# Kernel optimization log

Measured on AMD Instinct MI355X. Metric: run time of the kernel, lower is better.

Reference implementation:

```python
import jax, jax.numpy as jnp
import numpy as np

B, S, D, KC = 32, 4096, 64, 256  # batch*heads, seq_len, head_dim, compressed dim


def setup_inputs() -> dict:
    key = jax.random.key(0)
    ks = jax.random.split(key, 7)
    return {
        "Q": jax.random.normal(ks[0], (B, S, D), dtype=jnp.float32),
        "K": jax.random.normal(ks[1], (B, S, D), dtype=jnp.float32),
        "V": jax.random.normal(ks[2], (B, S, D), dtype=jnp.float32),
        "E_w": jax.random.normal(ks[3], (KC, S), dtype=jnp.float32) * (1.0 / np.sqrt(S)),
        "E_b": jax.random.normal(ks[4], (KC,), dtype=jnp.float32) * 0.01,
        "F_w": jax.random.normal(ks[5], (KC, S), dtype=jnp.float32) * (1.0 / np.sqrt(S)),
        "F_b": jax.random.normal(ks[6], (KC,), dtype=jnp.float32) * 0.01,
    }


def reference(Q, K, V, E_w, E_b, F_w, F_b):
    # K: [B,S,D] -> transpose -> [B,D,S]; E proj over seq axis -> [B,D,KC]
    Ke = jnp.einsum("bsd,ks->bdk", K, E_w) + E_b  # [B, D, KC]
    # scores: Q @ E(K) -> [B, S, KC], scaled by sqrt(head_dim)
    scale = jnp.sqrt(jnp.asarray(D, dtype=Q.dtype))
    P = jnp.einsum("bsd,bdk->bsk", Q, Ke) / scale
    # causal mask: torch.triu(ones(S, KC)) keeps (i, j) where j >= i
    i = jnp.arange(S)[:, None]
    j = jnp.arange(KC)[None, :]
    keep = j >= i  # [S, KC]
    P = jnp.where(keep[None, :, :], P, jnp.asarray(-1e10, dtype=P.dtype))
    P = jax.nn.softmax(P, axis=-1)  # dropout p=0.0 -> identity
    # V: [B,S,D] -> [B,D,S]; F proj -> [B,D,KC]; transpose -> [B,KC,D]
    Vf = jnp.einsum("bsd,ks->bkd", V, F_w) + F_b[None, :, None]  # [B, KC, D]
    out = jnp.einsum("bsk,bkd->bsd", P, Vf)  # [B, S, D]
    return out
```

## Files before the change

kernel.cpp:

```cpp
#include <hip/hip_runtime.h>
#include <hip/hip_bf16.h>
#include <math.h>

#define NB  32
#define NS  4096
#define ND  64
#define NKC 256

#define BK   128
#define ASA  132
#define ASB  132

#define QSTR  72
#define PBSTR 264
#define VSTR  264

typedef __attribute__((ext_vector_type(8))) short short8;
typedef __attribute__((ext_vector_type(4))) float f32x4;

__device__ __forceinline__ short f2bf(float f) {
    union { float f; unsigned u; } v; v.f = f;
    return (short)((v.u + 0x7FFFu + ((v.u >> 16) & 1u)) >> 16);
}

__global__ __launch_bounds__(256) void prep(
    const float* __restrict__ Ew, const float* __restrict__ Fw,
    short* __restrict__ EwB, short* __restrict__ FwB)
{
    const int gid = blockIdx.x * 256 + threadIdx.x;
    const int half = (NKC * NS) / 8;
    const float* src = (gid < half) ? Ew : Fw;
    short* dst       = (gid < half) ? EwB : FwB;
    const int i8 = (gid < half) ? gid : gid - half;
    float4 a = *(const float4*)&src[(size_t)i8 * 8];
    float4 c = *(const float4*)&src[(size_t)i8 * 8 + 4];
    short8 w;
    w[0] = f2bf(a.x); w[1] = f2bf(a.y); w[2] = f2bf(a.z); w[3] = f2bf(a.w);
    w[4] = f2bf(c.x); w[5] = f2bf(c.y); w[6] = f2bf(c.z); w[7] = f2bf(c.w);
    *(short8*)&dst[(size_t)i8 * 8] = w;
}

template <typename AT>
__global__ __launch_bounds__(256) void proj_gemm(
    const AT* __restrict__ EwX, const AT* __restrict__ FwX,
    const float* __restrict__ K, const float* __restrict__ V,
    float* __restrict__ KeT, float* __restrict__ Vf)
{
    const int bid = blockIdx.x;
    const int r8 = bid & 7, mt = (bid >> 3) & 3, G = bid >> 5;
    const int g  = G * 8 + r8, b = g >> 1, mm = g & 1;

    const AT* __restrict__ Ab    = mm ? FwX : EwX;
    const float* __restrict__ Bg = mm ? V   : K;
    float* __restrict__ Cout     = mm ? Vf  : KeT;

    const int t = threadIdx.x, wave = t >> 6, lane = t & 63;
    const int lm = lane & 15, g4 = lane >> 4;
    __shared__ short As[64 * ASA];
    __shared__ short Bs[64 * ASB];
    const size_t bBase = (size_t)b * NS * ND;
    const size_t aBase = (size_t)mt * 64 * NS;
    const int rA = t >> 4, jA = t & 15;
    const int dB = t & 31, sB = t >> 5;

    f32x4 acc[4];
#pragma unroll
    for (int nt = 0; nt < 4; ++nt) acc[nt] = (f32x4){0.f, 0.f, 0.f, 0.f};

    short8 pa[4];
    float4 paf[8];
    float2 pb[16];

#pragma unroll
    for (int i = 0; i < 4; ++i) {
        if constexpr (sizeof(AT) == 2) {
            pa[i] = *(const short8*)&Ab[aBase + (size_t)(i * 16 + rA) * NS + jA * 8];
        } else {
            paf[2 * i]     = *(const float4*)&Ab[aBase + (size_t)(i * 16 + rA) * NS + jA * 8];
            paf[2 * i + 1] = *(const float4*)&Ab[aBase + (size_t)(i * 16 + rA) * NS + jA * 8 + 4];
        }
    }
#pragma unroll
    for (int h = 0; h < 2; ++h)
#pragma unroll
        for (int i = 0; i < 8; ++i)
            pb[h * 8 + i] = *(const float2*)&Bg[bBase + (size_t)(h * 64 + sB * 8 + i) * ND + dB * 2];

    for (int s0 = 0; s0 < NS; s0 += BK) {
#pragma unroll
        for (int i = 0; i < 4; ++i) {
            if constexpr (sizeof(AT) == 2) {
                *(short8*)&As[(i * 16 + rA) * ASA + jA * 8] = pa[i];
            } else {
                short8 w;
                w[0] = f2bf(paf[2 * i].x);     w[1] = f2bf(paf[2 * i].y);
                w[2] = f2bf(paf[2 * i].z);     w[3] = f2bf(paf[2 * i].w);
                w[4] = f2bf(paf[2 * i + 1].x); w[5] = f2bf(paf[2 * i + 1].y);
                w[6] = f2bf(paf[2 * i + 1].z); w[7] = f2bf(paf[2 * i + 1].w);
                *(short8*)&As[(i * 16 + rA) * ASA + jA * 8] = w;
            }
        }
#pragma unroll
        for (int h = 0; h < 2; ++h) {
            short8 w0, w1;
#pragma unroll
            for (int i = 0; i < 8; ++i) {
                w0[i] = f2bf(pb[h * 8 + i].x);
                w1[i] = f2bf(pb[h * 8 + i].y);
            }
            *(short8*)&Bs[(dB * 2 + 0) * ASB + h * 64 + sB * 8] = w0;
            *(short8*)&Bs[(dB * 2 + 1) * ASB + h * 64 + sB * 8] = w1;
        }
        __syncthreads();

        if (s0 + BK < NS) {
            const int sn = s0 + BK;
#pragma unroll
            for (int i = 0; i < 4; ++i) {
                if constexpr (sizeof(AT) == 2) {
                    pa[i] = *(const short8*)&Ab[aBase + (size_t)(i * 16 + rA) * NS + sn + jA * 8];
                } else {
                    paf[2 * i]     = *(const float4*)&Ab[aBase + (size_t)(i * 16 + rA) * NS + sn + jA * 8];
                    paf[2 * i + 1] = *(const float4*)&Ab[aBase + (size_t)(i * 16 + rA) * NS + sn + jA * 8 + 4];
                }
            }
#pragma unroll
            for (int h = 0; h < 2; ++h)
#pragma unroll
                for (int i = 0; i < 8; ++i)
                    pb[h * 8 + i] = *(const float2*)&Bg[bBase + (size_t)(sn + h * 64 + sB * 8 + i) * ND + dB * 2];
        }

#pragma unroll
        for (int ks = 0; ks < BK; ks += 32) {
            short8 aF = *(const short8*)&As[(wave * 16 + lm) * ASA + ks + g4 * 8];
#pragma unroll
            for (int nt = 0; nt < 4; ++nt) {
                short8 bF = *(const short8*)&Bs[(nt * 16 + lm) * ASB + ks + g4 * 8];
                acc[nt] = __builtin_amdgcn_mfma_f32_16x16x32_bf16(aF, bF, acc[nt], 0, 0, 0);
            }
        }
        __syncthreads();
    }

#pragma unroll
    for (int nt = 0; nt < 4; ++nt)
#pragma unroll
        for (int rr = 0; rr < 4; ++rr) {
            int kc = mt * 64 + wave * 16 + g4 * 4 + rr;
            Cout[((size_t)b * NKC + kc) * ND + nt * 16 + lm] = acc[nt][rr];
        }
}

__global__ __launch_bounds__(256) void attn_fused(
    const float* __restrict__ Q,  const float* __restrict__ KeT,
    const float* __restrict__ Vf, const float* __restrict__ Eb,
    const float* __restrict__ Fb, float* __restrict__ out)
{
    const int x = blockIdx.x, b = blockIdx.y, t = threadIdx.x;

    if (x >= 8) {
        __shared__ float pq[16][64];
        __shared__ float mv[64];
        const int kg = t >> 4, dq = t & 15;
        float4 s4 = (float4){0.f, 0.f, 0.f, 0.f};
        for (int p = 0; p < 16; ++p) {
            int k = p * 16 + kg;
            float4 v = *(const float4*)&Vf[((size_t)b * NKC + k) * ND + dq * 4];
            float fb = Fb[k];
            s4.x += v.x + fb; s4.y += v.y + fb; s4.z += v.z + fb; s4.w += v.w + fb;
        }
        *(float4*)&pq[kg][dq * 4] = s4;
        __syncthreads();
        if (t < 64) {
            float m = 0.f;
#pragma unroll
            for (int i = 0; i < 16; ++i) m += pq[i][t];
            mv[t] = m * (1.f / 256.f);
        }
        __syncthreads();
        const int r0 = 256 + (x - 8) * 64;
#pragma unroll
        for (int i = 0; i < 4; ++i) {
            int idx = i * 256 + t, row = idx >> 4, q = idx & 15;
            *(float4*)&out[((size_t)b * NS + r0 + row) * ND + q * 4] =
                *(const float4*)&mv[q * 4];
        }
        return;
    }

    const int s0 = x * 32;
    const int wave = t >> 6, lane = t & 63, lm = lane & 15, g = lane >> 4;
    __shared__ short Qs[32 * QSTR];
    __shared__ short PsB[32 * PBSTR];
    __shared__ short VfT[64 * VSTR];
    __shared__ float rsums[32][4];

    {
        int row = t >> 3, dq = t & 7;
        size_t off = ((size_t)b * NS + s0 + row) * ND + dq * 8;
        float4 q0 = *(const float4*)&Q[off], q1 = *(const float4*)&Q[off + 4];
        short8 w;
        w[0] = f2bf(q0.x); w[1] = f2bf(q0.y); w[2] = f2bf(q0.z); w[3] = f2bf(q0.w);
        w[4] = f2bf(q1.x); w[5] = f2bf(q1.y); w[6] = f2bf(q1.z); w[7] = f2bf(q1.w);
        *(short8*)&Qs[row * QSTR + dq * 8] = w;
    }
    {
        const int dB = t & 31, sB = t >> 5;
#pragma unroll
        for (int pass = 0; pass < 4; ++pass) {
            int kb = pass * 64 + sB * 8;
            float2 v[8]; float fb[8];
#pragma unroll
            for (int i = 0; i < 8; ++i) {
                v[i]  = *(const float2*)&Vf[((size_t)b * NKC + kb + i) * ND + dB * 2];
                fb[i] = Fb[kb + i];
            }
            short8 w0, w1;
#pragma unroll
            for (int i = 0; i < 8; ++i) {
                w0[i] = f2bf(v[i].x + fb[i]);
                w1[i] = f2bf(v[i].y + fb[i]);
            }
            *(short8*)&VfT[(dB * 2 + 0) * VSTR + kb] = w0;
            *(short8*)&VfT[(dB * 2 + 1) * VSTR + kb] = w1;
        }
    }
    __syncthreads();

    f32x4 accP[2][4];
#pragma unroll
    for (int rt = 0; rt < 2; ++rt)
#pragma unroll
        for (int kk = 0; kk < 4; ++kk) accP[rt][kk] = (f32x4){0.f, 0.f, 0.f, 0.f};
#pragma unroll
    for (int kk = 0; kk < 4; ++kk) {
        int kt = wave * 4 + kk;
        float ebv = Eb[kt * 16 + lm];
#pragma unroll
        for (int ks2 = 0; ks2 < 2; ++ks2) {
            const float* kp = &KeT[((size_t)b * NKC + kt * 16 + lm) * ND + ks2 * 32 + g * 8];
            float4 c0 = *(const float4*)kp, c1 = *(const float4*)(kp + 4);
            short8 bf;
            bf[0] = f2bf(c0.x + ebv); bf[1] = f2bf(c0.y + ebv);
            bf[2] = f2bf(c0.z + ebv); bf[3] = f2bf(c0.w + ebv);
            bf[4] = f2bf(c1.x + ebv); bf[5] = f2bf(c1.y + ebv);
            bf[6] = f2bf(c1.z + ebv); bf[7] = f2bf(c1.w + ebv);
#pragma unroll
            for (int rt = 0; rt < 2; ++rt) {
                short8 aq = *(const short8*)&Qs[(rt * 16 + lm) * QSTR + ks2 * 32 + g * 8];
                accP[rt][kk] = __builtin_amdgcn_mfma_f32_16x16x32_bf16(aq, bf, accP[rt][kk], 0, 0, 0);
            }
        }
    }
#pragma unroll
    for (int rt = 0; rt < 2; ++rt)
#pragma unroll
        for (int r = 0; r < 4; ++r) {
            float s = 0.f;
            int rowg = s0 + rt * 16 + g * 4 + r;
#pragma unroll
            for (int kk = 0; kk < 4; ++kk) {
                int col = wave * 64 + kk * 16 + lm;
                float e = (col >= rowg) ? __expf(accP[rt][kk][r] * 0.125f) : 0.f;
                accP[rt][kk][r] = e;
                s += e;
            }
#pragma unroll
            for (int off = 1; off <= 8; off <<= 1) s += __shfl_xor(s, off, 64);
            if (lm == 0) rsums[rt * 16 + g * 4 + r][wave] = s;
        }
    __syncthreads();
#pragma unroll
    for (int rt = 0; rt < 2; ++rt)
#pragma unroll
        for (int r = 0; r < 4; ++r) {
            float4 rs = *(const float4*)&rsums[rt * 16 + g * 4 + r][0];
            float inv = 1.f / (rs.x + rs.y + rs.z + rs.w);
#pragma unroll
            for (int kk = 0; kk < 4; ++kk)
                PsB[(rt * 16 + g * 4 + r) * PBSTR + wave * 64 + kk * 16 + lm] =
                    f2bf(accP[rt][kk][r] * inv);
        }
    __syncthreads();

    f32x4 oa[2];
    oa[0] = (f32x4){0.f, 0.f, 0.f, 0.f};
    oa[1] = (f32x4){0.f, 0.f, 0.f, 0.f};
    for (int ks = x; ks < 8; ++ks) {
        short8 bv = *(const short8*)&VfT[(wave * 16 + lm) * VSTR + ks * 32 + g * 8];
#pragma unroll
        for (int rt = 0; rt < 2; ++rt) {
            short8 av = *(const short8*)&PsB[(rt * 16 + lm) * PBSTR + ks * 32 + g * 8];
            oa[rt] = __builtin_amdgcn_mfma_f32_16x16x32_bf16(av, bv, oa[rt], 0, 0, 0);
        }
    }
#pragma unroll
    for (int rt = 0; rt < 2; ++rt)
#pragma unroll
        for (int r = 0; r < 4; ++r)
            out[((size_t)b * NS + s0 + rt * 16 + g * 4 + r) * ND + wave * 16 + lm] = oa[rt][r];
}

extern "C" void kernel_launch(void* const* d_in, const int* in_sizes, int n_in,
                              void* d_out, int out_size, void* d_ws, size_t ws_size,
                              hipStream_t stream) {
    (void)in_sizes; (void)n_in; (void)out_size;
    const float* Q  = (const float*)d_in[0];
    const float* K  = (const float*)d_in[1];
    const float* V  = (const float*)d_in[2];
    const float* Ew = (const float*)d_in[3];
    const float* Eb = (const float*)d_in[4];
    const float* Fw = (const float*)d_in[5];
    const float* Fb = (const float*)d_in[6];
    float* out = (float*)d_out;

    const size_t nKe = (size_t)NB * NKC * ND;
    float* KeT = (float*)d_ws;
    float* Vf  = KeT + nKe;

    if (ws_size >= 8u * 1024 * 1024) {
        short* EwB = (short*)(Vf + nKe);
        short* FwB = EwB + (size_t)NKC * NS;
        prep<<<dim3(1024), 256, 0, stream>>>(Ew, Fw, EwB, FwB);
        proj_gemm<short><<<dim3(256), 256, 0, stream>>>(EwB, FwB, K, V, KeT, Vf);
    } else {
        proj_gemm<float><<<dim3(256), 256, 0, stream>>>(Ew, Fw, K, V, KeT, Vf);
    }
    attn_fused<<<dim3(68, NB), 256, 0, stream>>>(Q, KeT, Vf, Eb, Fb, out);
}
```

Before: 195.3 us.

## Retile projection GEMM into 32x64 tiles with 512-thread blocks

The projection GEMM now has each block compute a 32-row slice of the compressed dimension instead of 64. Blocks grow to 512 threads (8 waves), and each wave owns a single 16x16 output tile. The grid doubles to 512 blocks, which raises parallelism and occupancy and shrinks per-thread register state. The cost is that each K/V chunk is loaded and converted to bf16 by twice as many blocks, and each wave issues only one MFMA per shared-memory fragment load.

```diff
diff --git a/kernel.cpp b/kernel.cpp
--- a/kernel.cpp
+++ b/kernel.cpp
@@ -41,13 +41,13 @@
 }
 
 template <typename AT>
-__global__ __launch_bounds__(256) void proj_gemm(
+__global__ __launch_bounds__(512, 4) void proj_gemm(
     const AT* __restrict__ EwX, const AT* __restrict__ FwX,
     const float* __restrict__ K, const float* __restrict__ V,
     float* __restrict__ KeT, float* __restrict__ Vf)
 {
     const int bid = blockIdx.x;
-    const int r8 = bid & 7, mt = (bid >> 3) & 3, G = bid >> 5;
+    const int r8 = bid & 7, mt = (bid >> 3) & 7, G = bid >> 6;
     const int g  = G * 8 + r8, b = g >> 1, mm = g & 1;
 
     const AT* __restrict__ Ab    = mm ? FwX : EwX;
@@ -56,100 +56,77 @@
 
     const int t = threadIdx.x, wave = t >> 6, lane = t & 63;
     const int lm = lane & 15, g4 = lane >> 4;
-    __shared__ short As[64 * ASA];
+    const int kcT = wave & 1, dT = wave >> 1;
+    __shared__ short As[32 * ASA];
     __shared__ short Bs[64 * ASB];
     const size_t bBase = (size_t)b * NS * ND;
-    const size_t aBase = (size_t)mt * 64 * NS;
+    const size_t aBase = (size_t)mt * 32 * NS;
     const int rA = t >> 4, jA = t & 15;
     const int dB = t & 31, sB = t >> 5;
 
-    f32x4 acc[4];
-#pragma unroll
-    for (int nt = 0; nt < 4; ++nt) acc[nt] = (f32x4){0.f, 0.f, 0.f, 0.f};
-
-    short8 pa[4];
-    float4 paf[8];
-    float2 pb[16];
-
-#pragma unroll
-    for (int i = 0; i < 4; ++i) {
+    f32x4 acc = (f32x4){0.f, 0.f, 0.f, 0.f};
+
+    short8 pa;
+    float4 paf[2];
+    float2 pb[8];
+
+    if constexpr (sizeof(AT) == 2) {
+        pa = *(const short8*)&Ab[aBase + (size_t)rA * NS + jA * 8];
+    } else {
+        paf[0] = *(const float4*)&Ab[aBase + (size_t)rA * NS + jA * 8];
+        paf[1] = *(const float4*)&Ab[aBase + (size_t)rA * NS + jA * 8 + 4];
+    }
+#pragma unroll
+    for (int i = 0; i < 8; ++i)
+        pb[i] = *(const float2*)&Bg[bBase + (size_t)(sB * 8 + i) * ND + dB * 2];
+
+    for (int s0 = 0; s0 < NS; s0 += BK) {
         if constexpr (sizeof(AT) == 2) {
-            pa[i] = *(const short8*)&Ab[aBase + (size_t)(i * 16 + rA) * NS + jA * 8];
+            *(short8*)&As[rA * ASA + jA * 8] = pa;
         } else {
-            paf[2 * i]     = *(const float4*)&Ab[aBase + (size_t)(i * 16 + rA) * NS + jA * 8];
-            paf[2 * i + 1] = *(const float4*)&Ab[aBase + (size_t)(i * 16 + rA) * NS + jA * 8 + 4];
-        }
-    }
-#pragma unroll
-    for (int h = 0; h < 2; ++h)
-#pragma unroll
-        for (int i = 0; i < 8; ++i)
-            pb[h * 8 + i] = *(const float2*)&Bg[bBase + (size_t)(h * 64 + sB * 8 + i) * ND + dB * 2];
-
-    for (int s0 = 0; s0 < NS; s0 += BK) {
-#pragma unroll
-        for (int i = 0; i < 4; ++i) {
-            if constexpr (sizeof(AT) == 2) {
-                *(short8*)&As[(i * 16 + rA) * ASA + jA * 8] = pa[i];
-            } else {
-                short8 w;
-                w[0] = f2bf(paf[2 * i].x);     w[1] = f2bf(paf[2 * i].y);
-                w[2] = f2bf(paf[2 * i].z);     w[3] = f2bf(paf[2 * i].w);
-                w[4] = f2bf(paf[2 * i + 1].x); w[5] = f2bf(paf[2 * i + 1].y);
-                w[6] = f2bf(paf[2 * i + 1].z); w[7] = f2bf(paf[2 * i + 1].w);
-                *(short8*)&As[(i * 16 + rA) * ASA + jA * 8] = w;
-            }
-        }
-#pragma unroll
-        for (int h = 0; h < 2; ++h) {
+            short8 w;
+            w[0] = f2bf(paf[0].x); w[1] = f2bf(paf[0].y);
+            w[2] = f2bf(paf[0].z); w[3] = f2bf(paf[0].w);
+            w[4] = f2bf(paf[1].x); w[5] = f2bf(paf[1].y);
+            w[6] = f2bf(paf[1].z); w[7] = f2bf(paf[1].w);
+            *(short8*)&As[rA * ASA + jA * 8] = w;
+        }
+        {
             short8 w0, w1;
 #pragma unroll
-            for (int i = 0; i < 8; ++i) {
-                w0[i] = f2bf(pb[h * 8 + i].x);
-                w1[i] = f2bf(pb[h * 8 + i].y);
-            }
-            *(short8*)&Bs[(dB * 2 + 0) * ASB + h * 64 + sB * 8] = w0;
-            *(short8*)&Bs[(dB * 2 + 1) * ASB + h * 64 + sB * 8] = w1;
+            for (int i = 0; i < 8; ++i) { w0[i] = f2bf(pb[i].x); w1[i] = f2bf(pb[i].y); }
+            *(short8*)&Bs[(dB * 2 + 0) * ASB + sB * 8] = w0;
+            *(short8*)&Bs[(dB * 2 + 1) * ASB + sB * 8] = w1;
         }
         __syncthreads();
 
         if (s0 + BK < NS) {
             const int sn = s0 + BK;
-#pragma unroll
-            for (int i = 0; i < 4; ++i) {
-                if constexpr (sizeof(AT) == 2) {
-                    pa[i] = *(const short8*)&Ab[aBase + (size_t)(i * 16 + rA) * NS + sn + jA * 8];
-                } else {
-                    paf[2 * i]     = *(const float4*)&Ab[aBase + (size_t)(i * 16 + rA) * NS + sn + jA * 8];
-                    paf[2 * i + 1] = *(const float4*)&Ab[aBase + (size_t)(i * 16 + rA) * NS + sn + jA * 8 + 4];
-                }
-            }
-#pragma unroll
-            for (int h = 0; h < 2; ++h)
-#pragma unroll
-                for (int i = 0; i < 8; ++i)
-                    pb[h * 8 + i] = *(const float2*)&Bg[bBase + (size_t)(sn + h * 64 + sB * 8 + i) * ND + dB * 2];
+            if constexpr (sizeof(AT) == 2) {
+                pa = *(const short8*)&Ab[aBase + (size_t)rA * NS + sn + jA * 8];
+            } else {
+                paf[0] = *(const float4*)&Ab[aBase + (size_t)rA * NS + sn + jA * 8];
+                paf[1] = *(const float4*)&Ab[aBase + (size_t)rA * NS + sn + jA * 8 + 4];
+            }
+#pragma unroll
+            for (int i = 0; i < 8; ++i)
+                pb[i] = *(const float2*)&Bg[bBase + (size_t)(sn + sB * 8 + i) * ND + dB * 2];
         }
 
 #pragma unroll
         for (int ks = 0; ks < BK; ks += 32) {
-            short8 aF = *(const short8*)&As[(wave * 16 + lm) * ASA + ks + g4 * 8];
-#pragma unroll
-            for (int nt = 0; nt < 4; ++nt) {
-                short8 bF = *(const short8*)&Bs[(nt * 16 + lm) * ASB + ks + g4 * 8];
-                acc[nt] = __builtin_amdgcn_mfma_f32_16x16x32_bf16(aF, bF, acc[nt], 0, 0, 0);
-            }
+            short8 aF = *(const short8*)&As[(kcT * 16 + lm) * ASA + ks + g4 * 8];
+            short8 bF = *(const short8*)&Bs[(dT * 16 + lm) * ASB + ks + g4 * 8];
+            acc = __builtin_amdgcn_mfma_f32_16x16x32_bf16(aF, bF, acc, 0, 0, 0);
         }
         __syncthreads();
     }
 
 #pragma unroll
-    for (int nt = 0; nt < 4; ++nt)
-#pragma unroll
-        for (int rr = 0; rr < 4; ++rr) {
-            int kc = mt * 64 + wave * 16 + g4 * 4 + rr;
-            Cout[((size_t)b * NKC + kc) * ND + nt * 16 + lm] = acc[nt][rr];
-        }
+    for (int rr = 0; rr < 4; ++rr) {
+        int kc = mt * 32 + kcT * 16 + g4 * 4 + rr;
+        Cout[((size_t)b * NKC + kc) * ND + dT * 16 + lm] = acc[rr];
+    }
 }
 
 __global__ __launch_bounds__(256) void attn_fused(
@@ -323,9 +300,9 @@
         short* EwB = (short*)(Vf + nKe);
         short* FwB = EwB + (size_t)NKC * NS;
         prep<<<dim3(1024), 256, 0, stream>>>(Ew, Fw, EwB, FwB);
-        proj_gemm<short><<<dim3(256), 256, 0, stream>>>(EwB, FwB, K, V, KeT, Vf);
+        proj_gemm<short><<<dim3(512), 512, 0, stream>>>(EwB, FwB, K, V, KeT, Vf);
     } else {
-        proj_gemm<float><<<dim3(256), 256, 0, stream>>>(Ew, Fw, K, V, KeT, Vf);
+        proj_gemm<float><<<dim3(512), 512, 0, stream>>>(Ew, Fw, K, V, KeT, Vf);
     }
     attn_fused<<<dim3(68, NB), 256, 0, stream>>>(Q, KeT, Vf, Eb, Fb, out);
 }
```

Result: no change. 193.3 us (-1.1%).

## Split-K the projection GEMM across sequence halves and add a reduction pass

Applied to the files above, without the earlier changes.

The projection GEMM is split along the sequence (reduction) axis into two halves, which doubles the grid from 256 to 512 blocks so more of the GPU's compute units get work. Each half writes partial KeT/Vf results into separate workspace buffers, and a new reduce2 kernel sums them before the attention kernel runs. The cost is an extra kernel launch, extra global traffic for the partial buffers, and a larger workspace requirement before the bf16 prep path is taken. A launch-bounds occupancy hint of 2 blocks per CU is also added.

```diff
diff --git a/kernel.cpp b/kernel.cpp
--- a/kernel.cpp
+++ b/kernel.cpp
@@ -8,6 +8,7 @@
 #define NKC 256
 
 #define BK   128
+#define KHALF 2048
 #define ASA  132
 #define ASB  132
 
@@ -41,18 +42,20 @@
 }
 
 template <typename AT>
-__global__ __launch_bounds__(256) void proj_gemm(
+__global__ __launch_bounds__(256, 2) void proj_sk(
     const AT* __restrict__ EwX, const AT* __restrict__ FwX,
     const float* __restrict__ K, const float* __restrict__ V,
-    float* __restrict__ KeT, float* __restrict__ Vf)
+    float* __restrict__ KeTa, float* __restrict__ Vfa,
+    float* __restrict__ KeTb, float* __restrict__ Vfb)
 {
     const int bid = blockIdx.x;
-    const int r8 = bid & 7, mt = (bid >> 3) & 3, G = bid >> 5;
-    const int g  = G * 8 + r8, b = g >> 1, mm = g & 1;
+    const int r8 = bid & 7, mt = (bid >> 3) & 3, gq = bid >> 5;
+    const int grp = gq * 8 + r8;
+    const int kh = grp & 1, mm = (grp >> 1) & 1, b = grp >> 2;
 
     const AT* __restrict__ Ab    = mm ? FwX : EwX;
     const float* __restrict__ Bg = mm ? V   : K;
-    float* __restrict__ Cout     = mm ? Vf  : KeT;
+    float* __restrict__ Cout = kh ? (mm ? Vfb : KeTb) : (mm ? Vfa : KeTa);
 
     const int t = threadIdx.x, wave = t >> 6, lane = t & 63;
     const int lm = lane & 15, g4 = lane >> 4;
@@ -71,22 +74,24 @@
     float4 paf[8];
     float2 pb[16];
 
+    const int sBeg = kh * KHALF, sEnd = sBeg + KHALF;
+
 #pragma unroll
     for (int i = 0; i < 4; ++i) {
         if constexpr (sizeof(AT) == 2) {
-            pa[i] = *(const short8*)&Ab[aBase + (size_t)(i * 16 + rA) * NS + jA * 8];
+            pa[i] = *(const short8*)&Ab[aBase + (size_t)(i * 16 + rA) * NS + sBeg + jA * 8];
         } else {
-            paf[2 * i]     = *(const float4*)&Ab[aBase + (size_t)(i * 16 + rA) * NS + jA * 8];
-            paf[2 * i + 1] = *(const float4*)&Ab[aBase + (size_t)(i * 16 + rA) * NS + jA * 8 + 4];
+            paf[2 * i]     = *(const float4*)&Ab[aBase + (size_t)(i * 16 + rA) * NS + sBeg + jA * 8];
+            paf[2 * i + 1] = *(const float4*)&Ab[aBase + (size_t)(i * 16 + rA) * NS + sBeg + jA * 8 + 4];
         }
     }
 #pragma unroll
     for (int h = 0; h < 2; ++h)
 #pragma unroll
         for (int i = 0; i < 8; ++i)
-            pb[h * 8 + i] = *(const float2*)&Bg[bBase + (size_t)(h * 64 + sB * 8 + i) * ND + dB * 2];
-
-    for (int s0 = 0; s0 < NS; s0 += BK) {
+            pb[h * 8 + i] = *(const float2*)&Bg[bBase + (size_t)(sBeg + h * 64 + sB * 8 + i) * ND + dB * 2];
+
+    for (int s0 = sBeg; s0 < sEnd; s0 += BK) {
 #pragma unroll
         for (int i = 0; i < 4; ++i) {
             if constexpr (sizeof(AT) == 2) {
@@ -113,7 +118,7 @@
         }
         __syncthreads();
 
-        if (s0 + BK < NS) {
+        if (s0 + BK < sEnd) {
             const int sn = s0 + BK;
 #pragma unroll
             for (int i = 0; i < 4; ++i) {
@@ -150,6 +155,14 @@
             int kc = mt * 64 + wave * 16 + g4 * 4 + rr;
             Cout[((size_t)b * NKC + kc) * ND + nt * 16 + lm] = acc[nt][rr];
         }
+}
+
+__global__ __launch_bounds__(256) void reduce2(
+    float4* __restrict__ Areg, const float4* __restrict__ Breg)
+{
+    const int gid = blockIdx.x * 256 + threadIdx.x;
+    float4 a = Areg[gid], c = Breg[gid];
+    Areg[gid] = (float4){a.x + c.x, a.y + c.y, a.z + c.z, a.w + c.w};
 }
 
 __global__ __launch_bounds__(256) void attn_fused(
@@ -316,16 +329,23 @@
     float* out = (float*)d_out;
 
     const size_t nKe = (size_t)NB * NKC * ND;
-    float* KeT = (float*)d_ws;
-    float* Vf  = KeT + nKe;
-
-    if (ws_size >= 8u * 1024 * 1024) {
-        short* EwB = (short*)(Vf + nKe);
+    float* base = (float*)d_ws;
+    float* KeTa = base;
+    float* Vfa  = base + nKe;
+    float* KeTb = base + 2 * nKe;
+    float* Vfb  = base + 3 * nKe;
+
+    if (ws_size >= 12u * 1024 * 1024) {
+        short* EwB = (short*)(base + 4 * nKe);
         short* FwB = EwB + (size_t)NKC * NS;
         prep<<<dim3(1024), 256, 0, stream>>>(Ew, Fw, EwB, FwB);
-        proj_gemm<short><<<dim3(256), 256, 0, stream>>>(EwB, FwB, K, V, KeT, Vf);
+        proj_sk<short><<<dim3(512), 256, 0, stream>>>(EwB, FwB, K, V,
+                                                      KeTa, Vfa, KeTb, Vfb);
     } else {
-        proj_gemm<float><<<dim3(256), 256, 0, stream>>>(Ew, Fw, K, V, KeT, Vf);
-    }
-    attn_fused<<<dim3(68, NB), 256, 0, stream>>>(Q, KeT, Vf, Eb, Fb, out);
-}
+        proj_sk<float><<<dim3(512), 256, 0, stream>>>(Ew, Fw, K, V,
+                                                      KeTa, Vfa, KeTb, Vfb);
+    }
+    reduce2<<<dim3(1024), 256, 0, stream>>>((float4*)base,
+                                            (const float4*)(base + 2 * nKe));
+    attn_fused<<<dim3(68, NB), 256, 0, stream>>>(Q, KeTa, Vfa, Eb, Fb, out);
+}
```

After: 185.6 us. 1.05x faster.
